# Performance work log

Measured on AMD Instinct MI355X. Metric: run time of the kernel, lower is better.

## Reference

```python
import jax, jax.numpy as jnp
import numpy as np

SIZE = 4096
DOWN = SIZE // 16  # reduction_factor = 16 -> 256
N_TASKS = 16
BATCH = 2048
INIT_STD = 0.01


def setup_inputs() -> dict:
    key = jax.random.key(0)
    k_x, k_t, k_wd, k_wu = jax.random.split(key, 4)
    x = jax.random.normal(k_x, (BATCH, SIZE), dtype=jnp.float32)
    task_id = jax.random.randint(k_t, (BATCH,), 0, N_TASKS)
    # Stacked per-task adapter params (init: normal(std=0.01) weights, zero bias)
    Wd = jax.random.normal(k_wd, (N_TASKS, SIZE, DOWN), dtype=jnp.float32) * INIT_STD
    bd = jnp.zeros((N_TASKS, DOWN), dtype=jnp.float32)
    Wu = jax.random.normal(k_wu, (N_TASKS, DOWN, SIZE), dtype=jnp.float32) * INIT_STD
    bu = jnp.zeros((N_TASKS, SIZE), dtype=jnp.float32)
    return {"x": x, "task_id": task_id, "Wd": Wd, "bd": bd, "Wu": Wu, "bu": bu}


def reference(x, task_id, Wd, bd, Wu, bu):
    # Down-projection for all tasks, then select each sample's routed task.
    # [B, T, DOWN] is small (B*T*256), cheaper than gathering [B, SIZE, DOWN] weights.
    down_all = jnp.einsum('bd,tdh->bth', x, Wd) + bd[None]
    down = jnp.take_along_axis(down_all, task_id[:, None, None], axis=1)[:, 0]  # [B, DOWN]
    act = jax.nn.silu(down)
    # Up-projection for all tasks, select routed task. [B, T, SIZE]
    up_all = jnp.einsum('bh,thd->btd', act, Wu) + bu[None]
    up = jnp.take_along_axis(up_all, task_id[:, None, None], axis=1)[:, 0]  # [B, SIZE]
    return x + up  # residual=True (default)
```

## Files before the change

kernel.cpp:

```cpp
#include <hip/hip_runtime.h>

#define BATCH 2048
#define SIZE 4096
#define DOWN 256
#define NTASK 16
#define KC 16
#define KCHUNK (SIZE / KC)

typedef _Float16 half8 __attribute__((ext_vector_type(8)));
typedef float floatx4 __attribute__((ext_vector_type(4)));

__device__ __forceinline__ int imin(int a, int b) { return a < b ? a : b; }

__global__ __launch_bounds__(256) void sort_kernel(const int* __restrict__ task_id,
                                                   int* __restrict__ taskOff,
                                                   int* __restrict__ sortedIdx,
                                                   int* __restrict__ taskOfPos) {
    __shared__ int cnt[NTASK];
    __shared__ int base[NTASK + 1];
    __shared__ int cur[NTASK];
    int tid = threadIdx.x;
    if (tid < NTASK) cnt[tid] = 0;
    __syncthreads();
    for (int i = tid; i < BATCH; i += 256) atomicAdd(&cnt[task_id[i]], 1);
    __syncthreads();
    if (tid == 0) {
        int s = 0;
        for (int t = 0; t < NTASK; t++) { base[t] = s; s += cnt[t]; }
        base[NTASK] = s;
    }
    __syncthreads();
    if (tid < NTASK) { cur[tid] = base[tid]; taskOff[tid] = base[tid]; }
    if (tid == 0) taskOff[NTASK] = BATCH;
    __syncthreads();
    for (int i = tid; i < BATCH; i += 256) {
        int t = task_id[i];
        int p = atomicAdd(&cur[t], 1);
        sortedIdx[p] = i;
        taskOfPos[p] = t;
    }
}

__global__ __launch_bounds__(256) void gemm1_kernel(const float* __restrict__ x,
                                                    const float* __restrict__ Wd,
                                                    const int* __restrict__ taskOff,
                                                    const int* __restrict__ sortedIdx,
                                                    _Float16* __restrict__ partial) {
    int task = blockIdx.x, kc = blockIdx.y;
    int rowStart = taskOff[task];
    int nrows = taskOff[task + 1] - rowStart;
    if (nrows <= 0) return;

    __shared__ half8 A_lds[8][65];
    __shared__ half8 B_lds[8][256];

    int tid = threadIdx.x;
    int wave = tid >> 6, lane = tid & 63, quad = lane >> 4, l15 = lane & 15;
    int kbase0 = kc * KCHUNK;
    const float* Wdt = Wd + (size_t)task * SIZE * DOWN;

    for (int r0 = 0; r0 < nrows; r0 += 64) {
        floatx4 acc[4][4];
#pragma unroll
        for (int mi = 0; mi < 4; mi++)
#pragma unroll
            for (int ni = 0; ni < 4; ni++) acc[mi][ni] = (floatx4){0.f, 0.f, 0.f, 0.f};

        int arow = tid >> 2;
        int asrc = sortedIdx[rowStart + imin(r0 + arow, nrows - 1)];
        const float* xrow = x + (size_t)asrc * SIZE;

        for (int kb = 0; kb < KCHUNK; kb += 64) {
            int kglob = kbase0 + kb;
            __syncthreads();
#pragma unroll
            for (int j = 0; j < 2; j++) {
                int kg = ((tid & 3) << 1) | j;
                const float* src = xrow + kglob + kg * 8;
                float4 f0 = *(const float4*)(src);
                float4 f1 = *(const float4*)(src + 4);
                half8 h;
                h[0] = (_Float16)f0.x; h[1] = (_Float16)f0.y;
                h[2] = (_Float16)f0.z; h[3] = (_Float16)f0.w;
                h[4] = (_Float16)f1.x; h[5] = (_Float16)f1.y;
                h[6] = (_Float16)f1.z; h[7] = (_Float16)f1.w;
                A_lds[kg][arow] = h;
            }
#pragma unroll
            for (int kg = 0; kg < 8; kg++) {
                half8 h;
#pragma unroll
                for (int i = 0; i < 8; i++)
                    h[i] = (_Float16)Wdt[(size_t)(kglob + kg * 8 + i) * DOWN + tid];
                B_lds[kg][tid] = h;
            }
            __syncthreads();
#pragma unroll
            for (int ks = 0; ks < 2; ks++) {
                int kg = ks * 4 + quad;
                half8 a[4], b[4];
#pragma unroll
                for (int i = 0; i < 4; i++) a[i] = A_lds[kg][i * 16 + l15];
#pragma unroll
                for (int i = 0; i < 4; i++) b[i] = B_lds[kg][wave * 64 + i * 16 + l15];
#pragma unroll
                for (int mi = 0; mi < 4; mi++)
#pragma unroll
                    for (int ni = 0; ni < 4; ni++)
                        acc[mi][ni] = __builtin_amdgcn_mfma_f32_16x16x32_f16(
                            a[mi], b[ni], acc[mi][ni], 0, 0, 0);
            }
        }
#pragma unroll
        for (int mi = 0; mi < 4; mi++) {
#pragma unroll
            for (int reg = 0; reg < 4; reg++) {
                int r = r0 + mi * 16 + quad * 4 + reg;
                if (r < nrows) {
                    size_t rowoff = ((size_t)kc * BATCH + (rowStart + r)) * DOWN;
#pragma unroll
                    for (int ni = 0; ni < 4; ni++) {
                        int h = wave * 64 + ni * 16 + l15;
                        partial[rowoff + h] = (_Float16)acc[mi][ni][reg];
                    }
                }
            }
        }
    }
}

__global__ __launch_bounds__(256) void silu_kernel(const _Float16* __restrict__ partial,
                                                   const float* __restrict__ bd,
                                                   const int* __restrict__ taskOfPos,
                                                   _Float16* __restrict__ act) {
    int idx = blockIdx.x * 256 + threadIdx.x;
    int s = idx >> 8, h = idx & 255;
    float v = bd[taskOfPos[s] * DOWN + h];
#pragma unroll
    for (int kc = 0; kc < KC; kc++) v += (float)partial[((size_t)kc * BATCH + s) * DOWN + h];
    float sv = v / (1.0f + __expf(-v));
    act[idx] = (_Float16)sv;
}

__global__ __launch_bounds__(256) void gemm2_kernel(const _Float16* __restrict__ act,
                                                    const float* __restrict__ Wu,
                                                    const float* __restrict__ bu,
                                                    const float* __restrict__ x,
                                                    const int* __restrict__ taskOff,
                                                    const int* __restrict__ sortedIdx,
                                                    float* __restrict__ out) {
    int task = blockIdx.x, nt = blockIdx.y;
    int rowStart = taskOff[task];
    int nrows = taskOff[task + 1] - rowStart;
    if (nrows <= 0) return;

    __shared__ half8 A_lds[8][129];
    __shared__ half8 B_lds[8][128];

    int tid = threadIdx.x;
    int wave = tid >> 6, lane = tid & 63, quad = lane >> 4, l15 = lane & 15;
    int wm = wave >> 1, wn = wave & 1;
    int ncol0 = nt * 128;
    const float* Wut = Wu + (size_t)task * DOWN * SIZE;

    for (int r0 = 0; r0 < nrows; r0 += 128) {
        floatx4 acc[4][4];
#pragma unroll
        for (int mi = 0; mi < 4; mi++)
#pragma unroll
            for (int ni = 0; ni < 4; ni++) acc[mi][ni] = (floatx4){0.f, 0.f, 0.f, 0.f};

        int arow = tid >> 1;
        int s_a = rowStart + imin(r0 + arow, nrows - 1);
        const _Float16* actrow = act + (size_t)s_a * DOWN;

        for (int kb = 0; kb < DOWN; kb += 64) {
            __syncthreads();
#pragma unroll
            for (int j = 0; j < 4; j++) {
                int kg = ((tid & 1) << 2) | j;
                A_lds[kg][arow] = *(const half8*)(actrow + kb + kg * 8);
            }
            int nl = tid & 127;
#pragma unroll
            for (int j = 0; j < 4; j++) {
                int kg = ((tid >> 7) << 2) | j;
                half8 h;
#pragma unroll
                for (int i = 0; i < 8; i++)
                    h[i] = (_Float16)Wut[(size_t)(kb + kg * 8 + i) * SIZE + ncol0 + nl];
                B_lds[kg][nl] = h;
            }
            __syncthreads();
#pragma unroll
            for (int ks = 0; ks < 2; ks++) {
                int kg = ks * 4 + quad;
                half8 a[4], b[4];
#pragma unroll
                for (int i = 0; i < 4; i++) a[i] = A_lds[kg][wm * 64 + i * 16 + l15];
#pragma unroll
                for (int i = 0; i < 4; i++) b[i] = B_lds[kg][wn * 64 + i * 16 + l15];
#pragma unroll
                for (int mi = 0; mi < 4; mi++)
#pragma unroll
                    for (int ni = 0; ni < 4; ni++)
                        acc[mi][ni] = __builtin_amdgcn_mfma_f32_16x16x32_f16(
                            a[mi], b[ni], acc[mi][ni], 0, 0, 0);
            }
        }
#pragma unroll
        for (int mi = 0; mi < 4; mi++) {
#pragma unroll
            for (int reg = 0; reg < 4; reg++) {
                int r = r0 + wm * 64 + mi * 16 + quad * 4 + reg;
                if (r < nrows) {
                    int b = sortedIdx[rowStart + r];
                    const float* xr = x + (size_t)b * SIZE;
                    float* outr = out + (size_t)b * SIZE;
#pragma unroll
                    for (int ni = 0; ni < 4; ni++) {
                        int n = ncol0 + wn * 64 + ni * 16 + l15;
                        outr[n] = acc[mi][ni][reg] + bu[task * SIZE + n] + xr[n];
                    }
                }
            }
        }
    }
}

extern "C" void kernel_launch(void* const* d_in, const int* in_sizes, int n_in,
                              void* d_out, int out_size, void* d_ws, size_t ws_size,
                              hipStream_t stream) {
    const float* x       = (const float*)d_in[0];
    const int*   task_id = (const int*)d_in[1];
    const float* Wd      = (const float*)d_in[2];
    const float* bd      = (const float*)d_in[3];
    const float* Wu      = (const float*)d_in[4];
    const float* bu      = (const float*)d_in[5];
    float* out = (float*)d_out;

    _Float16* partial = (_Float16*)d_out;
    _Float16* act     = (_Float16*)d_ws;
    int* taskOff   = (int*)(act + (size_t)BATCH * DOWN);
    int* sortedIdx = taskOff + 32;
    int* taskOfPos = sortedIdx + BATCH;

    sort_kernel<<<1, 256, 0, stream>>>(task_id, taskOff, sortedIdx, taskOfPos);
    gemm1_kernel<<<dim3(NTASK, KC), 256, 0, stream>>>(x, Wd, taskOff, sortedIdx, partial);
    silu_kernel<<<(BATCH * DOWN) / 256, 256, 0, stream>>>(partial, bd, taskOfPos, act);
    gemm2_kernel<<<dim3(NTASK, SIZE / 128), 256, 0, stream>>>(act, Wu, bu, x, taskOff,
                                                              sortedIdx, out);
}
```

Before: 246.7 us.

## Vectorize weight loads, prefetch into registers, swizzle LDS, split gemm1 rows

Both GEMM kernels now fetch weight tiles as float4 vectors into registers before the barrier, then transpose and convert them to fp16 into LDS at XOR-swizzled column positions. The goal is to replace scalar strided global loads, overlap global latency with the previous barrier, and reduce LDS bank conflicts. gemm1 splits each task's row tiles across two blocks to double parallelism, and both kernels get a launch_bounds occupancy hint. The silu kernel processes 8 elements per thread with vector loads and stores, and gemm2's grid is reordered so column tiles of the same task launch adjacently. These changes raise register pressure and add swizzle index arithmetic.

```diff
diff --git a/kernel.cpp b/kernel.cpp
--- a/kernel.cpp
+++ b/kernel.cpp
@@ -11,6 +11,7 @@
 typedef float floatx4 __attribute__((ext_vector_type(4)));
 
 __device__ __forceinline__ int imin(int a, int b) { return a < b ? a : b; }
+__device__ __forceinline__ int uswz(int n) { return n ^ ((n >> 3) & 7); }
 
 __global__ __launch_bounds__(256) void sort_kernel(const int* __restrict__ task_id,
                                                    int* __restrict__ taskOff,
@@ -41,12 +42,12 @@
     }
 }
 
-__global__ __launch_bounds__(256) void gemm1_kernel(const float* __restrict__ x,
-                                                    const float* __restrict__ Wd,
-                                                    const int* __restrict__ taskOff,
-                                                    const int* __restrict__ sortedIdx,
-                                                    _Float16* __restrict__ partial) {
-    int task = blockIdx.x, kc = blockIdx.y;
+__global__ __launch_bounds__(256, 2) void gemm1_kernel(const float* __restrict__ x,
+                                                       const float* __restrict__ Wd,
+                                                       const int* __restrict__ taskOff,
+                                                       const int* __restrict__ sortedIdx,
+                                                       _Float16* __restrict__ partial) {
+    int task = blockIdx.x >> 1, z = blockIdx.x & 1, kc = blockIdx.y;
     int rowStart = taskOff[task];
     int nrows = taskOff[task + 1] - rowStart;
     if (nrows <= 0) return;
@@ -59,7 +60,11 @@
     int kbase0 = kc * KCHUNK;
     const float* Wdt = Wd + (size_t)task * SIZE * DOWN;
 
-    for (int r0 = 0; r0 < nrows; r0 += 64) {
+    int bswz[4];
+#pragma unroll
+    for (int i = 0; i < 4; i++) bswz[i] = uswz(wave * 64 + i * 16 + l15);
+
+    for (int r0 = z * 64; r0 < nrows; r0 += 128) {
         floatx4 acc[4][4];
 #pragma unroll
         for (int mi = 0; mi < 4; mi++)
@@ -72,27 +77,43 @@
 
         for (int kb = 0; kb < KCHUNK; kb += 64) {
             int kglob = kbase0 + kb;
-            __syncthreads();
+            floatx4 fa[2][2];
 #pragma unroll
             for (int j = 0; j < 2; j++) {
                 int kg = ((tid & 3) << 1) | j;
                 const float* src = xrow + kglob + kg * 8;
-                float4 f0 = *(const float4*)(src);
-                float4 f1 = *(const float4*)(src + 4);
+                fa[j][0] = *(const floatx4*)(src);
+                fa[j][1] = *(const floatx4*)(src + 4);
+            }
+            floatx4 fb[2][8];
+#pragma unroll
+            for (int s = 0; s < 2; s++) {
+                int kg = s * 4 + wave;
+                const float* src = Wdt + (size_t)(kglob + kg * 8) * DOWN + lane * 4;
+#pragma unroll
+                for (int j = 0; j < 8; j++) fb[s][j] = *(const floatx4*)(src + (size_t)j * DOWN);
+            }
+            __syncthreads();
+#pragma unroll
+            for (int j = 0; j < 2; j++) {
+                int kg = ((tid & 3) << 1) | j;
                 half8 h;
-                h[0] = (_Float16)f0.x; h[1] = (_Float16)f0.y;
-                h[2] = (_Float16)f0.z; h[3] = (_Float16)f0.w;
-                h[4] = (_Float16)f1.x; h[5] = (_Float16)f1.y;
-                h[6] = (_Float16)f1.z; h[7] = (_Float16)f1.w;
+                h[0] = (_Float16)fa[j][0][0]; h[1] = (_Float16)fa[j][0][1];
+                h[2] = (_Float16)fa[j][0][2]; h[3] = (_Float16)fa[j][0][3];
+                h[4] = (_Float16)fa[j][1][0]; h[5] = (_Float16)fa[j][1][1];
+                h[6] = (_Float16)fa[j][1][2]; h[7] = (_Float16)fa[j][1][3];
                 A_lds[kg][arow] = h;
             }
 #pragma unroll
-            for (int kg = 0; kg < 8; kg++) {
-                half8 h;
-#pragma unroll
-                for (int i = 0; i < 8; i++)
-                    h[i] = (_Float16)Wdt[(size_t)(kglob + kg * 8 + i) * DOWN + tid];
-                B_lds[kg][tid] = h;
+            for (int s = 0; s < 2; s++) {
+                int kg = s * 4 + wave;
+#pragma unroll
+                for (int i = 0; i < 4; i++) {
+                    half8 h;
+#pragma unroll
+                    for (int j = 0; j < 8; j++) h[j] = (_Float16)fb[s][j][i];
+                    B_lds[kg][uswz(lane * 4 + i)] = h;
+                }
             }
             __syncthreads();
 #pragma unroll
@@ -102,7 +123,7 @@
 #pragma unroll
                 for (int i = 0; i < 4; i++) a[i] = A_lds[kg][i * 16 + l15];
 #pragma unroll
-                for (int i = 0; i < 4; i++) b[i] = B_lds[kg][wave * 64 + i * 16 + l15];
+                for (int i = 0; i < 4; i++) b[i] = B_lds[kg][bswz[i]];
 #pragma unroll
                 for (int mi = 0; mi < 4; mi++)
 #pragma unroll
@@ -134,22 +155,37 @@
                                                    const int* __restrict__ taskOfPos,
                                                    _Float16* __restrict__ act) {
     int idx = blockIdx.x * 256 + threadIdx.x;
-    int s = idx >> 8, h = idx & 255;
-    float v = bd[taskOfPos[s] * DOWN + h];
-#pragma unroll
-    for (int kc = 0; kc < KC; kc++) v += (float)partial[((size_t)kc * BATCH + s) * DOWN + h];
-    float sv = v / (1.0f + __expf(-v));
-    act[idx] = (_Float16)sv;
-}
-
-__global__ __launch_bounds__(256) void gemm2_kernel(const _Float16* __restrict__ act,
-                                                    const float* __restrict__ Wu,
-                                                    const float* __restrict__ bu,
-                                                    const float* __restrict__ x,
-                                                    const int* __restrict__ taskOff,
-                                                    const int* __restrict__ sortedIdx,
-                                                    float* __restrict__ out) {
-    int task = blockIdx.x, nt = blockIdx.y;
+    int s = idx >> 5;
+    int h = (idx & 31) * 8;
+    int t = taskOfPos[s];
+    floatx4 b0 = *(const floatx4*)(bd + t * DOWN + h);
+    floatx4 b1 = *(const floatx4*)(bd + t * DOWN + h + 4);
+    float v[8];
+    v[0] = b0[0]; v[1] = b0[1]; v[2] = b0[2]; v[3] = b0[3];
+    v[4] = b1[0]; v[5] = b1[1]; v[6] = b1[2]; v[7] = b1[3];
+#pragma unroll
+    for (int kc = 0; kc < KC; kc++) {
+        half8 p = *(const half8*)(partial + ((size_t)kc * BATCH + s) * DOWN + h);
+#pragma unroll
+        for (int j = 0; j < 8; j++) v[j] += (float)p[j];
+    }
+    half8 o;
+#pragma unroll
+    for (int j = 0; j < 8; j++) {
+        float sv = v[j] / (1.0f + __expf(-v[j]));
+        o[j] = (_Float16)sv;
+    }
+    *(half8*)(act + (size_t)s * DOWN + h) = o;
+}
+
+__global__ __launch_bounds__(256, 2) void gemm2_kernel(const _Float16* __restrict__ act,
+                                                       const float* __restrict__ Wu,
+                                                       const float* __restrict__ bu,
+                                                       const float* __restrict__ x,
+                                                       const int* __restrict__ taskOff,
+                                                       const int* __restrict__ sortedIdx,
+                                                       float* __restrict__ out) {
+    int nt = blockIdx.x, task = blockIdx.y;
     int rowStart = taskOff[task];
     int nrows = taskOff[task + 1] - rowStart;
     if (nrows <= 0) return;
@@ -163,6 +199,11 @@
     int ncol0 = nt * 128;
     const float* Wut = Wu + (size_t)task * DOWN * SIZE;
 
+    int bswz[4];
+#pragma unroll
+    for (int i = 0; i < 4; i++) bswz[i] = uswz(wn * 64 + i * 16 + l15);
+    int kgB = tid >> 5, nfB = tid & 31;
+
     for (int r0 = 0; r0 < nrows; r0 += 128) {
         floatx4 acc[4][4];
 #pragma unroll
@@ -175,21 +216,28 @@
         const _Float16* actrow = act + (size_t)s_a * DOWN;
 
         for (int kb = 0; kb < DOWN; kb += 64) {
-            __syncthreads();
+            half8 ha[4];
 #pragma unroll
             for (int j = 0; j < 4; j++) {
                 int kg = ((tid & 1) << 2) | j;
-                A_lds[kg][arow] = *(const half8*)(actrow + kb + kg * 8);
-            }
-            int nl = tid & 127;
+                ha[j] = *(const half8*)(actrow + kb + kg * 8);
+            }
+            floatx4 fb[8];
+            const float* src = Wut + (size_t)(kb + kgB * 8) * SIZE + ncol0 + nfB * 4;
+#pragma unroll
+            for (int j = 0; j < 8; j++) fb[j] = *(const floatx4*)(src + (size_t)j * SIZE);
+            __syncthreads();
 #pragma unroll
             for (int j = 0; j < 4; j++) {
-                int kg = ((tid >> 7) << 2) | j;
+                int kg = ((tid & 1) << 2) | j;
+                A_lds[kg][arow] = ha[j];
+            }
+#pragma unroll
+            for (int i = 0; i < 4; i++) {
                 half8 h;
 #pragma unroll
-                for (int i = 0; i < 8; i++)
-                    h[i] = (_Float16)Wut[(size_t)(kb + kg * 8 + i) * SIZE + ncol0 + nl];
-                B_lds[kg][nl] = h;
+                for (int j = 0; j < 8; j++) h[j] = (_Float16)fb[j][i];
+                B_lds[kgB][uswz(nfB * 4 + i)] = h;
             }
             __syncthreads();
 #pragma unroll
@@ -199,7 +247,7 @@
 #pragma unroll
                 for (int i = 0; i < 4; i++) a[i] = A_lds[kg][wm * 64 + i * 16 + l15];
 #pragma unroll
-                for (int i = 0; i < 4; i++) b[i] = B_lds[kg][wn * 64 + i * 16 + l15];
+                for (int i = 0; i < 4; i++) b[i] = B_lds[kg][bswz[i]];
 #pragma unroll
                 for (int mi = 0; mi < 4; mi++)
 #pragma unroll
@@ -246,8 +294,8 @@
     int* taskOfPos = sortedIdx + BATCH;
 
     sort_kernel<<<1, 256, 0, stream>>>(task_id, taskOff, sortedIdx, taskOfPos);
-    gemm1_kernel<<<dim3(NTASK, KC), 256, 0, stream>>>(x, Wd, taskOff, sortedIdx, partial);
-    silu_kernel<<<(BATCH * DOWN) / 256, 256, 0, stream>>>(partial, bd, taskOfPos, act);
-    gemm2_kernel<<<dim3(NTASK, SIZE / 128), 256, 0, stream>>>(act, Wu, bu, x, taskOff,
+    gemm1_kernel<<<dim3(NTASK * 2, KC), 256, 0, stream>>>(x, Wd, taskOff, sortedIdx, partial);
+    silu_kernel<<<(BATCH * DOWN / 8) / 256, 256, 0, stream>>>(partial, bd, taskOfPos, act);
+    gemm2_kernel<<<dim3(SIZE / 128, NTASK), 256, 0, stream>>>(act, Wu, bu, x, taskOff,
                                                               sortedIdx, out);
 }
```

After: 236.1 us, median of 2. 1.04x faster.
